# Kernel tuning notes

Hardware: AMD Instinct MI355X
Metric: run time of the kernel (lower is better)

Reference implementation:

```python
import jax, jax.numpy as jnp
import numpy as np

B, T, D = 64, 512, 256
K = 8192  # num_embeddings


def setup_inputs() -> dict:
    key = jax.random.key(0)
    k1, k2 = jax.random.split(key)
    inputs = jax.random.normal(k1, (B, T, D), dtype=jnp.float32)
    # nn.Embedding weight init: uniform(-1/K, 1/K)
    emb_weight = jax.random.uniform(k2, (K, D), dtype=jnp.float32, minval=-1.0 / K, maxval=1.0 / K)
    return {"inputs": inputs, "emb_weight": emb_weight}


def reference(inputs, emb_weight):
    d = emb_weight.shape[1]
    flat = inputs.reshape(-1, d)  # [N, D]
    # squared L2 distances to all codes: [N, K]
    distances = (
        jnp.sum(flat * flat, axis=1, keepdims=True)
        + jnp.sum(emb_weight * emb_weight, axis=1)
        - 2.0 * jnp.matmul(flat, emb_weight.T)
    )
    encoding_indices = jnp.argmin(distances, axis=1)  # [N]
    # one-hot @ codebook == direct gather of nearest code
    quantized = emb_weight[encoding_indices].reshape(inputs.shape)
    e_latent_loss = jnp.mean((jax.lax.stop_gradient(quantized) - inputs) ** 2)
    q_latent_loss = jnp.mean((quantized - jax.lax.stop_gradient(inputs)) ** 2)
    loss = q_latent_loss + e_latent_loss
    # straight-through estimator
    quantized_st = inputs + jax.lax.stop_gradient(quantized - inputs)
    return quantized_st, loss, encoding_indices.reshape(inputs.shape[0], -1)
```

## Files before the change

kernel.cpp:

```cpp
#include <hip/hip_runtime.h>

#define N_ROWS 32768
#define DIM 256
#define N_CODES 8192
#define OUT_Q 8388608
#define OUT_LOSS 8388608
#define OUT_IDX 8388609
#define FLAG_GAP 7e-5f
#define CAND_CAP 262144

#define WS_AROW 0
#define WS_IDX  131072
#define WS_LIST 262144
#define WS_CNT  393216
#define WS_CCNT 393232
#define WS_S1   393472
#define WS_KEYS 524544
#define WS_PART 524544
#define WS_EIMG 1048576

typedef __attribute__((ext_vector_type(8))) short short8x;
typedef __attribute__((ext_vector_type(4))) float f32x4;
typedef unsigned long long u64;
#define AS1 __attribute__((address_space(1)))
#define AS3 __attribute__((address_space(3)))

__device__ __forceinline__ u64 umin64(u64 a, u64 b) { return a < b ? a : b; }
__device__ __forceinline__ u64 umax64(u64 a, u64 b) { return a > b ? a : b; }
__device__ __forceinline__ unsigned fkey(float f) {
    unsigned b = __float_as_uint(f);
    return b ^ (unsigned)(((int)b >> 31) | 0x80000000);
}
__device__ __forceinline__ float fkeyinv(unsigned u) {
    unsigned b = (u >> 31) ? (u ^ 0x80000000u) : ~u;
    return __uint_as_float(b);
}
__device__ __forceinline__ unsigned short bf16rne(float f) {
    unsigned u = __float_as_uint(f);
    return (unsigned short)((u + 0x7fff + ((u >> 16) & 1)) >> 16);
}
__device__ __forceinline__ void gload16(const void* g, void* l) {
    __builtin_amdgcn_global_load_lds((const AS1 unsigned int*)g, (AS3 unsigned int*)l, 16, 0, 0);
}

__global__ void vq_prepE(const float* __restrict__ E, char* __restrict__ Eimg) {
    int t = blockIdx.x * 256 + threadIdx.x;
    int cb = t >> 10;
    int u = t & 1023;
    int w = u >> 7, v = u & 127;
    int sub = v >> 5, c = (v >> 4) & 1, l15 = v & 15;
    int tile = cb >> 3, S = cb & 7;
    const float* src = E + (size_t)(tile * 256 + w * 32 + c * 16 + l15) * DIM + S * 32 + sub * 8;
    unsigned short h[8], l[8];
#pragma unroll
    for (int j = 0; j < 8; ++j) {
        float vv = src[j];
        h[j] = bf16rne(vv);
        float hf = __uint_as_float((unsigned)h[j] << 16);
        l[j] = bf16rne(vv - hf);
    }
    short8x H, L;
#pragma unroll
    for (int j = 0; j < 8; ++j) { H[j] = (short)h[j]; L[j] = (short)l[j]; }
    char* dst = Eimg + (size_t)cb * 32768 + w * 4096 + sub * 512 + c * 256 + l15 * 16;
    *(short8x*)dst = H;
    *(short8x*)(dst + 2048) = L;
}

__global__ void vq_rowA(const float* __restrict__ X, float* __restrict__ Arow) {
    int row = blockIdx.x * 4 + (threadIdx.x >> 6);
    int lane = threadIdx.x & 63;
    const float4 v = *((const float4*)(X + (size_t)row * DIM + lane * 4));
    double s = (double)v.x * v.x + (double)v.y * v.y + (double)v.z * v.z + (double)v.w * v.w;
#pragma unroll
    for (int m = 1; m < 64; m <<= 1) s += __shfl_xor(s, m, 64);
    if (lane == 0) Arow[row] = (float)s;
}

template <int MODE>
__global__ __launch_bounds__(512, 1) void vq_scan(
    const float* __restrict__ X, const char* __restrict__ Eimg,
    const float* __restrict__ Arow, int* __restrict__ ws_idx,
    int* __restrict__ flaglist, int* __restrict__ flagcnt,
    u64* __restrict__ keybuf, float* __restrict__ s1buf,
    unsigned* __restrict__ cand, int* __restrict__ candcnt) {
    __shared__ alignas(16) unsigned short Xs[32768];
    __shared__ alignas(16) unsigned short Eb[32768];
    __shared__ int rows_s[64];

    const int tid = threadIdx.x;
    const int lane = tid & 63, wv = tid >> 6;
    const int l15 = lane & 15, sub = lane >> 4;

    const int cnt = (MODE == 1) ? *flagcnt : 0;
    const int ntasks = (MODE == 1) ? ((cnt + 63) >> 6) * 8 : 0;

    char* const ebase = (char*)Eb + wv * 4096;
    const char* const eimgw = Eimg + wv * 4096;

    float r1v[4][4], r2v[4][4];
    int c1v[4][4];
    if constexpr (MODE == 0) {
#pragma unroll
        for (int f = 0; f < 4; ++f)
#pragma unroll
            for (int g = 0; g < 4; ++g) { r1v[f][g] = 3.4e38f; r2v[f][g] = 3.4e38f; c1v[f][g] = 0; }
    }

    int task = blockIdx.x;
    while (true) {
        int t0, t1, r0;
        if constexpr (MODE == 1) {
            if (task >= ntasks) break;
            int grp = task >> 3;
            int rng = task & 7;
            t0 = rng * 4; t1 = t0 + 4;
            r0 = 0;
            __syncthreads();
            if (tid < 64) {
                int s = grp * 64 + tid;
                rows_s[tid] = flaglist[s < cnt ? s : cnt - 1];
            }
            __syncthreads();
        } else {
            t0 = 0; t1 = 32;
            r0 = blockIdx.x * 64;
        }
        const int cend = t1 * 8;

        {
            const int ci = t0 * 8;
            const char* src = eimgw + (size_t)ci * 32768 + lane * 16;
            char* dst = ebase + (ci & 1) * 32768;
#pragma unroll
            for (int i = 0; i < 4; ++i) gload16(src + i * 1024, dst + i * 1024);
        }
#pragma unroll
        for (int i = 0; i < 4; ++i) {
            int ci = tid + i * 512;
            int q = ci >> 6, r = ci & 63;
            int grow = (MODE == 1) ? rows_s[r] : r0 + r;
            const float* src = X + (size_t)grow * DIM + q * 8;
            unsigned short h[8], l[8];
#pragma unroll
            for (int j = 0; j < 8; ++j) {
                float v = src[j];
                h[j] = bf16rne(v);
                float hf = __uint_as_float((unsigned)h[j] << 16);
                l[j] = bf16rne(v - hf);
            }
            short8x H, L;
#pragma unroll
            for (int j = 0; j < 8; ++j) { H[j] = (short)h[j]; L[j] = (short)l[j]; }
            *(short8x*)((char*)Xs + q * 1024 + r * 16) = H;
            *(short8x*)((char*)Xs + 32768 + q * 1024 + r * 16) = L;
        }

        float A_r[4][4], s1v[4][4];
        int rid[4][4];
#pragma unroll
        for (int f = 0; f < 4; ++f)
#pragma unroll
            for (int g = 0; g < 4; ++g) {
                int rr = (MODE == 1) ? rows_s[f * 16 + sub * 4 + g] : r0 + f * 16 + sub * 4 + g;
                A_r[f][g] = Arow[rr];
                if constexpr (MODE == 1) { s1v[f][g] = s1buf[rr]; rid[f][g] = rr; }
            }

        __syncthreads();

        for (int t = t0; t < t1; ++t) {
            f32x4 acc[4][2];
#pragma unroll
            for (int f = 0; f < 4; ++f)
#pragma unroll
                for (int c = 0; c < 2; ++c) acc[f][c] = (f32x4){0.f, 0.f, 0.f, 0.f};

#pragma unroll
            for (int S = 0; S < 8; ++S) {
                const int ci = t * 8 + S;
                if (ci + 1 < cend) {
                    const char* src = eimgw + (size_t)(ci + 1) * 32768 + lane * 16;
                    char* dst = ebase + ((ci + 1) & 1) * 32768;
#pragma unroll
                    for (int i = 0; i < 4; ++i) gload16(src + i * 1024, dst + i * 1024);
                    __builtin_amdgcn_sched_barrier(0);
                    asm volatile("s_waitcnt vmcnt(4)" ::: "memory");
                } else {
                    asm volatile("s_waitcnt vmcnt(0)" ::: "memory");
                }
                __builtin_amdgcn_sched_barrier(0);

                const char* xb = (const char*)Xs;
                const char* eb = ebase + (ci & 1) * 32768;
                short8x ah[4], al[4], ehh[2], ell[2];
#pragma unroll
                for (int f = 0; f < 4; ++f) {
                    int off = (S * 4 + sub) * 1024 + f * 256 + l15 * 16;
                    ah[f] = *(const short8x*)(xb + off);
                    al[f] = *(const short8x*)(xb + 32768 + off);
                }
#pragma unroll
                for (int c = 0; c < 2; ++c) {
                    int off = sub * 512 + c * 256 + l15 * 16;
                    ehh[c] = *(const short8x*)(eb + off);
                    ell[c] = *(const short8x*)(eb + 2048 + off);
                }
#pragma unroll
                for (int f = 0; f < 4; ++f)
#pragma unroll
                    for (int c = 0; c < 2; ++c) {
                        f32x4 a = acc[f][c];
                        a = __builtin_amdgcn_mfma_f32_16x16x32_bf16(al[f], ehh[c], a, 0, 0, 0);
                        a = __builtin_amdgcn_mfma_f32_16x16x32_bf16(ah[f], ell[c], a, 0, 0, 0);
                        a = __builtin_amdgcn_mfma_f32_16x16x32_bf16(ah[f], ehh[c], a, 0, 0, 0);
                        acc[f][c] = a;
                    }
            }

            const int cbase = t * 256 + wv * 32 + l15;
            if constexpr (MODE == 0) {
#pragma unroll
                for (int f = 0; f < 4; ++f)
#pragma unroll
                    for (int g = 0; g < 4; ++g) {
                        float v0 = fmaf(-2.0f, acc[f][0][g], A_r[f][g]);
                        float v1 = fmaf(-2.0f, acc[f][1][g], A_r[f][g]);
                        float tt1 = fminf(v0, v1), tt2 = fmaxf(v0, v1);
                        int tc1 = (v1 < v0) ? cbase + 16 : cbase;
                        bool upd = (tt1 < r1v[f][g]);
                        r2v[f][g] = upd ? fminf(r1v[f][g], tt2) : fminf(r2v[f][g], tt1);
                        c1v[f][g] = upd ? tc1 : c1v[f][g];
                        r1v[f][g] = upd ? tt1 : r1v[f][g];
                    }
            } else {
#pragma unroll
                for (int f = 0; f < 4; ++f)
#pragma unroll
                    for (int g = 0; g < 4; ++g) {
                        float thr = s1v[f][g] + FLAG_GAP;
#pragma unroll
                        for (int c = 0; c < 2; ++c) {
                            float v = fmaf(-2.0f, acc[f][c][g], A_r[f][g]);
                            if (v <= thr) {
                                int slot = atomicAdd(candcnt, 1);
                                if (slot < CAND_CAP)
                                    cand[slot] = ((unsigned)rid[f][g] << 13) |
                                                 (unsigned)(cbase + c * 16);
                            }
                        }
                    }
            }
        }

        if constexpr (MODE == 0) break;
        else task += gridDim.x;
    }

    if constexpr (MODE == 0) {
        __syncthreads();
        u64* red = (u64*)Xs;
#pragma unroll
        for (int f = 0; f < 4; ++f)
#pragma unroll
            for (int g = 0; g < 4; ++g) {
                u64 k1 = ((u64)fkey(r1v[f][g]) << 32) | (unsigned)c1v[f][g];
                u64 k2 = ((u64)fkey(r2v[f][g]) << 32);
#pragma unroll
                for (int m = 1; m < 16; m <<= 1) {
                    u64 o1 = __shfl_xor(k1, m, 64);
                    u64 o2 = __shfl_xor(k2, m, 64);
                    u64 mx = umax64(k1, o1);
                    k1 = umin64(k1, o1);
                    k2 = umin64(umin64(k2, o2), mx);
                }
                if (l15 == 0) {
                    int row64 = f * 16 + sub * 4 + g;
                    red[(wv * 64 + row64) * 2 + 0] = k1;
                    red[(wv * 64 + row64) * 2 + 1] = k2;
                }
            }
        __syncthreads();
        if (tid < 64) {
            u64 K1 = red[tid * 2 + 0], K2 = red[tid * 2 + 1];
#pragma unroll
            for (int w = 1; w < 8; ++w) {
                u64 o1 = red[(w * 64 + tid) * 2 + 0], o2 = red[(w * 64 + tid) * 2 + 1];
                u64 mx = umax64(K1, o1);
                K1 = umin64(K1, o1);
                K2 = umin64(umin64(K2, o2), mx);
            }
            int r = blockIdx.x * 64 + tid;
            ws_idx[r] = (int)(unsigned)(K1 & 0xffffffffull);
            float s1 = fkeyinv((unsigned)(K1 >> 32));
            float s2 = fkeyinv((unsigned)(K2 >> 32));
            s1buf[r] = s1;
            if (s2 - s1 < FLAG_GAP) {
                keybuf[r] = ~0ull;
                int slot = atomicAdd(flagcnt, 1);
                flaglist[slot] = r;
            }
        }
    }
}

__global__ void vq_refine_cand(const float* __restrict__ X, const float* __restrict__ E,
                               const float* __restrict__ Arow, u64* __restrict__ keybuf,
                               const unsigned* __restrict__ cand,
                               const int* __restrict__ candcnt) {
    int cnt2 = *candcnt;
    cnt2 = cnt2 < CAND_CAP ? cnt2 : CAND_CAP;
    const int gw = (blockIdx.x * 256 + threadIdx.x) >> 6;
    const int nw = gridDim.x * 4;
    const int lane = threadIdx.x & 63;
    for (int i = gw; i < cnt2; i += nw) {
        unsigned p = cand[i];
        int row = (int)(p >> 13), code = (int)(p & 8191);
        float4 xv = *(const float4*)(X + (size_t)row * DIM + lane * 4);
        float4 ev = *(const float4*)(E + (size_t)code * DIM + lane * 4);
        double s = (double)xv.x * ev.x + (double)xv.y * ev.y +
                   (double)xv.z * ev.z + (double)xv.w * ev.w;
#pragma unroll
        for (int m = 1; m < 64; m <<= 1) s += __shfl_xor(s, m, 64);
        if (lane == 0) {
            float m32 = (float)s;
            float scr = fmaf(-2.0f, m32, Arow[row]);
            u64 key = ((u64)fkey(scr) << 32) | (unsigned)code;
            atomicMin(keybuf + row, key);
        }
    }
}

__global__ void vq_apply(const u64* __restrict__ keybuf, const int* __restrict__ flaglist,
                         const int* __restrict__ flagcnt, int* __restrict__ ws_idx) {
    int s = blockIdx.x * 256 + threadIdx.x;
    if (s < *flagcnt) {
        int r = flaglist[s];
        u64 k = keybuf[r];
        if (k != ~0ull) ws_idx[r] = (int)(unsigned)(k & 0xffffffffull);
    }
}

__global__ void vq_out(const float* __restrict__ X, const float* __restrict__ E,
                       const int* __restrict__ ws_idx, float* __restrict__ out,
                       float* __restrict__ partials) {
    const int r = (blockIdx.x * 256 + threadIdx.x) >> 6;
    const int lane = threadIdx.x & 63;
    int idx = ws_idx[r];
    idx = idx < 0 ? 0 : (idx > N_CODES - 1 ? N_CODES - 1 : idx);
    float4 e = *((const float4*)(E + (size_t)idx * DIM + lane * 4));
    float4 x = *((const float4*)(X + (size_t)r * DIM + lane * 4));
    float dx = e.x - x.x, dy = e.y - x.y, dz = e.z - x.z, dw = e.w - x.w;
    float4 o;
    o.x = x.x + dx; o.y = x.y + dy; o.z = x.z + dz; o.w = x.w + dw;
    *((float4*)(out + (size_t)r * DIM + lane * 4)) = o;
    float s = dx * dx + dy * dy + dz * dz + dw * dw;
#pragma unroll
    for (int m = 1; m < 64; m <<= 1) s += __shfl_xor(s, m, 64);
    if (lane == 0) {
        partials[r] = s;
        out[OUT_IDX + r] = (float)idx;
    }
}

__global__ void vq_loss(const float* __restrict__ partials, float* __restrict__ out) {
    __shared__ double sred[4];
    double s = 0.0;
    for (int i = threadIdx.x; i < N_ROWS; i += 256) s += (double)partials[i];
#pragma unroll
    for (int m = 1; m < 64; m <<= 1) s += __shfl_xor(s, m, 64);
    if ((threadIdx.x & 63) == 0) sred[threadIdx.x >> 6] = s;
    __syncthreads();
    if (threadIdx.x == 0) {
        double t = sred[0] + sred[1] + sred[2] + sred[3];
        out[OUT_LOSS] = (float)(2.0 * t / (double)OUT_Q);
    }
}

extern "C" void kernel_launch(void* const* d_in, const int* in_sizes, int n_in,
                              void* d_out, int out_size, void* d_ws, size_t ws_size,
                              hipStream_t stream) {
    const float* X = (const float*)d_in[0];
    const float* E = (const float*)d_in[1];
    float* out = (float*)d_out;
    char* ws = (char*)d_ws;

    float* Arow = (float*)(ws + WS_AROW);
    int* idx = (int*)(ws + WS_IDX);
    int* list = (int*)(ws + WS_LIST);
    int* cnt = (int*)(ws + WS_CNT);
    int* ccnt = (int*)(ws + WS_CCNT);
    float* s1buf = (float*)(ws + WS_S1);
    u64* keys = (u64*)(ws + WS_KEYS);
    float* part = (float*)(ws + WS_PART);
    char* eimg = (ws_size >= (size_t)(WS_EIMG + 8 * 1024 * 1024)) ? (ws + WS_EIMG) : (char*)d_out;
    unsigned* cand = (unsigned*)((char*)d_out + (16 << 20));

    hipMemsetAsync(ws + WS_CNT, 0, 32, stream);
    vq_prepE<<<1024, 256, 0, stream>>>(E, eimg);
    vq_rowA<<<N_ROWS / 4, 256, 0, stream>>>(X, Arow);
    vq_scan<0><<<N_ROWS / 64, 512, 0, stream>>>(X, eimg, Arow, idx, list, cnt, keys, s1buf,
                                                cand, ccnt);
    vq_scan<1><<<512, 512, 0, stream>>>(X, eimg, Arow, idx, list, cnt, keys, s1buf, cand, ccnt);
    vq_refine_cand<<<1024, 256, 0, stream>>>(X, E, Arow, keys, cand, ccnt);
    vq_apply<<<128, 256, 0, stream>>>(keys, list, cnt, idx);
    vq_out<<<N_ROWS / 4, 256, 0, stream>>>(X, E, idx, out, part);
    vq_loss<<<1, 256, 0, stream>>>(part, out);
}
```

Before: 542.8 us.

## Load codebook fragments directly into registers instead of staging through LDS

The codebook image is re-laid out so each lane's MFMA B-operand fragment is contiguous. Each wave then reads its fragments from global memory straight into registers, with a one-step register prefetch in place of global_load_lds double buffering. This removes the 64KB LDS buffer, the LDS reads and the explicit vmcnt waits. In exchange, global load latency is hidden only by the compiler's scheduling of one chunk ahead, and register pressure goes up.

```diff
diff --git a/kernel.cpp b/kernel.cpp
--- a/kernel.cpp
+++ b/kernel.cpp
@@ -22,8 +22,6 @@
 typedef __attribute__((ext_vector_type(8))) short short8x;
 typedef __attribute__((ext_vector_type(4))) float f32x4;
 typedef unsigned long long u64;
-#define AS1 __attribute__((address_space(1)))
-#define AS3 __attribute__((address_space(3)))
 
 __device__ __forceinline__ u64 umin64(u64 a, u64 b) { return a < b ? a : b; }
 __device__ __forceinline__ u64 umax64(u64 a, u64 b) { return a > b ? a : b; }
@@ -39,18 +37,18 @@
     unsigned u = __float_as_uint(f);
     return (unsigned short)((u + 0x7fff + ((u >> 16) & 1)) >> 16);
 }
-__device__ __forceinline__ void gload16(const void* g, void* l) {
-    __builtin_amdgcn_global_load_lds((const AS1 unsigned int*)g, (AS3 unsigned int*)l, 16, 0, 0);
-}
 
 __global__ void vq_prepE(const float* __restrict__ E, char* __restrict__ Eimg) {
     int t = blockIdx.x * 256 + threadIdx.x;
-    int cb = t >> 10;
+    int ci = t >> 10;
     int u = t & 1023;
-    int w = u >> 7, v = u & 127;
-    int sub = v >> 5, c = (v >> 4) & 1, l15 = v & 15;
-    int tile = cb >> 3, S = cb & 7;
-    const float* src = E + (size_t)(tile * 256 + w * 32 + c * 16 + l15) * DIM + S * 32 + sub * 8;
+    int wv = u >> 7;
+    int v = u & 127;
+    int c = v >> 6, lane = v & 63;
+    int tile = ci >> 3, S = ci & 7;
+    int code = tile * 256 + wv * 32 + c * 16 + (lane & 15);
+    int k0 = S * 32 + (lane >> 4) * 8;
+    const float* src = E + (size_t)code * DIM + k0;
     unsigned short h[8], l[8];
 #pragma unroll
     for (int j = 0; j < 8; ++j) {
@@ -62,7 +60,7 @@
     short8x H, L;
 #pragma unroll
     for (int j = 0; j < 8; ++j) { H[j] = (short)h[j]; L[j] = (short)l[j]; }
-    char* dst = Eimg + (size_t)cb * 32768 + w * 4096 + sub * 512 + c * 256 + l15 * 16;
+    char* dst = Eimg + (size_t)ci * 32768 + wv * 4096 + c * 1024 + lane * 16;
     *(short8x*)dst = H;
     *(short8x*)(dst + 2048) = L;
 }
@@ -85,7 +83,6 @@
     u64* __restrict__ keybuf, float* __restrict__ s1buf,
     unsigned* __restrict__ cand, int* __restrict__ candcnt) {
     __shared__ alignas(16) unsigned short Xs[32768];
-    __shared__ alignas(16) unsigned short Eb[32768];
     __shared__ int rows_s[64];
 
     const int tid = threadIdx.x;
@@ -95,8 +92,7 @@
     const int cnt = (MODE == 1) ? *flagcnt : 0;
     const int ntasks = (MODE == 1) ? ((cnt + 63) >> 6) * 8 : 0;
 
-    char* const ebase = (char*)Eb + wv * 4096;
-    const char* const eimgw = Eimg + wv * 4096;
+    const char* const eimgw = Eimg + wv * 4096 + lane * 16;
 
     float r1v[4][4], r2v[4][4];
     int c1v[4][4];
@@ -128,12 +124,13 @@
         }
         const int cend = t1 * 8;
 
+        short8x pnh0, pnh1, pnl0, pnl1;
         {
-            const int ci = t0 * 8;
-            const char* src = eimgw + (size_t)ci * 32768 + lane * 16;
-            char* dst = ebase + (ci & 1) * 32768;
-#pragma unroll
-            for (int i = 0; i < 4; ++i) gload16(src + i * 1024, dst + i * 1024);
+            const char* p = eimgw + (size_t)(t0 * 8) * 32768;
+            pnh0 = *(const short8x*)p;
+            pnh1 = *(const short8x*)(p + 1024);
+            pnl0 = *(const short8x*)(p + 2048);
+            pnl1 = *(const short8x*)(p + 3072);
         }
 #pragma unroll
         for (int i = 0; i < 4; ++i) {
@@ -179,21 +176,17 @@
 #pragma unroll
             for (int S = 0; S < 8; ++S) {
                 const int ci = t * 8 + S;
+                short8x eh0 = pnh0, eh1 = pnh1, el0 = pnl0, el1 = pnl1;
                 if (ci + 1 < cend) {
-                    const char* src = eimgw + (size_t)(ci + 1) * 32768 + lane * 16;
-                    char* dst = ebase + ((ci + 1) & 1) * 32768;
-#pragma unroll
-                    for (int i = 0; i < 4; ++i) gload16(src + i * 1024, dst + i * 1024);
-                    __builtin_amdgcn_sched_barrier(0);
-                    asm volatile("s_waitcnt vmcnt(4)" ::: "memory");
-                } else {
-                    asm volatile("s_waitcnt vmcnt(0)" ::: "memory");
-                }
-                __builtin_amdgcn_sched_barrier(0);
+                    const char* p = eimgw + (size_t)(ci + 1) * 32768;
+                    pnh0 = *(const short8x*)p;
+                    pnh1 = *(const short8x*)(p + 1024);
+                    pnl0 = *(const short8x*)(p + 2048);
+                    pnl1 = *(const short8x*)(p + 3072);
+                }
 
                 const char* xb = (const char*)Xs;
-                const char* eb = ebase + (ci & 1) * 32768;
-                short8x ah[4], al[4], ehh[2], ell[2];
+                short8x ah[4], al[4];
 #pragma unroll
                 for (int f = 0; f < 4; ++f) {
                     int off = (S * 4 + sub) * 1024 + f * 256 + l15 * 16;
@@ -201,21 +194,18 @@
                     al[f] = *(const short8x*)(xb + 32768 + off);
                 }
 #pragma unroll
-                for (int c = 0; c < 2; ++c) {
-                    int off = sub * 512 + c * 256 + l15 * 16;
-                    ehh[c] = *(const short8x*)(eb + off);
-                    ell[c] = *(const short8x*)(eb + 2048 + off);
-                }
-#pragma unroll
-                for (int f = 0; f < 4; ++f)
-#pragma unroll
-                    for (int c = 0; c < 2; ++c) {
-                        f32x4 a = acc[f][c];
-                        a = __builtin_amdgcn_mfma_f32_16x16x32_bf16(al[f], ehh[c], a, 0, 0, 0);
-                        a = __builtin_amdgcn_mfma_f32_16x16x32_bf16(ah[f], ell[c], a, 0, 0, 0);
-                        a = __builtin_amdgcn_mfma_f32_16x16x32_bf16(ah[f], ehh[c], a, 0, 0, 0);
-                        acc[f][c] = a;
-                    }
+                for (int f = 0; f < 4; ++f) {
+                    f32x4 a0 = acc[f][0];
+                    a0 = __builtin_amdgcn_mfma_f32_16x16x32_bf16(al[f], eh0, a0, 0, 0, 0);
+                    a0 = __builtin_amdgcn_mfma_f32_16x16x32_bf16(ah[f], el0, a0, 0, 0, 0);
+                    a0 = __builtin_amdgcn_mfma_f32_16x16x32_bf16(ah[f], eh0, a0, 0, 0, 0);
+                    acc[f][0] = a0;
+                    f32x4 a1 = acc[f][1];
+                    a1 = __builtin_amdgcn_mfma_f32_16x16x32_bf16(al[f], eh1, a1, 0, 0, 0);
+                    a1 = __builtin_amdgcn_mfma_f32_16x16x32_bf16(ah[f], el1, a1, 0, 0, 0);
+                    a1 = __builtin_amdgcn_mfma_f32_16x16x32_bf16(ah[f], eh1, a1, 0, 0, 0);
+                    acc[f][1] = a1;
+                }
             }
 
             const int cbase = t * 256 + wv * 32 + l15;
```

Result: slower. 1.195 ms (+120.1%).

## Track top-3 in scan to shrink the rescan list for ambiguous rows

Applied to the files above, without the earlier changes.

The first scan now keeps the best three distances per row, together with the indices of the best two. For rows with a small top-2 gap it pushes both candidates straight into the refine list. Only rows whose third-best is also within a gap threshold go to the second (full-codebook) rescan, which should cut the number of rows rescanned. The rescan task split is also refined from 8 to 16 code ranges per row group. The cost is more registers and compare logic in the hot scan loop, and a heuristic gap threshold that could miss a true nearest code.

```diff
diff --git a/kernel.cpp b/kernel.cpp
--- a/kernel.cpp
+++ b/kernel.cpp
@@ -7,13 +7,13 @@
 #define OUT_LOSS 8388608
 #define OUT_IDX 8388609
 #define FLAG_GAP 7e-5f
+#define GAP3 1e-4f
 #define CAND_CAP 262144
 
 #define WS_AROW 0
 #define WS_IDX  131072
 #define WS_LIST 262144
 #define WS_CNT  393216
-#define WS_CCNT 393232
 #define WS_S1   393472
 #define WS_KEYS 524544
 #define WS_PART 524544
@@ -26,7 +26,6 @@
 #define AS3 __attribute__((address_space(3)))
 
 __device__ __forceinline__ u64 umin64(u64 a, u64 b) { return a < b ? a : b; }
-__device__ __forceinline__ u64 umax64(u64 a, u64 b) { return a > b ? a : b; }
 __device__ __forceinline__ unsigned fkey(float f) {
     unsigned b = __float_as_uint(f);
     return b ^ (unsigned)(((int)b >> 31) | 0x80000000);
@@ -41,6 +40,15 @@
 }
 __device__ __forceinline__ void gload16(const void* g, void* l) {
     __builtin_amdgcn_global_load_lds((const AS1 unsigned int*)g, (AS3 unsigned int*)l, 16, 0, 0);
+}
+__device__ __forceinline__ void triple_merge(u64& k1, u64& k2, u64& k3, u64 o1, u64 o2, u64 o3) {
+    bool c = o1 < k1;
+    u64 A1 = c ? o1 : k1, A2 = c ? o2 : k2, A3 = c ? o3 : k3;
+    u64 B1 = c ? k1 : o1, B2 = c ? k2 : o2;
+    bool d = B1 < A2;
+    k1 = A1;
+    k2 = d ? B1 : A2;
+    k3 = d ? umin64(A2, B2) : umin64(A3, B1);
 }
 
 __global__ void vq_prepE(const float* __restrict__ E, char* __restrict__ Eimg) {
@@ -83,7 +91,8 @@
     const float* __restrict__ Arow, int* __restrict__ ws_idx,
     int* __restrict__ flaglist, int* __restrict__ flagcnt,
     u64* __restrict__ keybuf, float* __restrict__ s1buf,
-    unsigned* __restrict__ cand, int* __restrict__ candcnt) {
+    unsigned* __restrict__ cand, int* __restrict__ candcnt,
+    int* __restrict__ list2, int* __restrict__ cnt2) {
     __shared__ alignas(16) unsigned short Xs[32768];
     __shared__ alignas(16) unsigned short Eb[32768];
     __shared__ int rows_s[64];
@@ -93,18 +102,21 @@
     const int l15 = lane & 15, sub = lane >> 4;
 
     const int cnt = (MODE == 1) ? *flagcnt : 0;
-    const int ntasks = (MODE == 1) ? ((cnt + 63) >> 6) * 8 : 0;
+    const int ntasks = (MODE == 1) ? ((cnt + 63) >> 6) * 16 : 0;
 
     char* const ebase = (char*)Eb + wv * 4096;
     const char* const eimgw = Eimg + wv * 4096;
 
-    float r1v[4][4], r2v[4][4];
-    int c1v[4][4];
+    float r1v[4][4], r2v[4][4], r3v[4][4];
+    int c1v[4][4], c2v[4][4];
     if constexpr (MODE == 0) {
 #pragma unroll
         for (int f = 0; f < 4; ++f)
 #pragma unroll
-            for (int g = 0; g < 4; ++g) { r1v[f][g] = 3.4e38f; r2v[f][g] = 3.4e38f; c1v[f][g] = 0; }
+            for (int g = 0; g < 4; ++g) {
+                r1v[f][g] = 3.4e38f; r2v[f][g] = 3.4e38f; r3v[f][g] = 3.4e38f;
+                c1v[f][g] = 0; c2v[f][g] = 0;
+            }
     }
 
     int task = blockIdx.x;
@@ -112,9 +124,9 @@
         int t0, t1, r0;
         if constexpr (MODE == 1) {
             if (task >= ntasks) break;
-            int grp = task >> 3;
-            int rng = task & 7;
-            t0 = rng * 4; t1 = t0 + 4;
+            int grp = task >> 4;
+            int rng = task & 15;
+            t0 = rng * 2; t1 = t0 + 2;
             r0 = 0;
             __syncthreads();
             if (tid < 64) {
@@ -226,12 +238,23 @@
                     for (int g = 0; g < 4; ++g) {
                         float v0 = fmaf(-2.0f, acc[f][0][g], A_r[f][g]);
                         float v1 = fmaf(-2.0f, acc[f][1][g], A_r[f][g]);
-                        float tt1 = fminf(v0, v1), tt2 = fmaxf(v0, v1);
-                        int tc1 = (v1 < v0) ? cbase + 16 : cbase;
-                        bool upd = (tt1 < r1v[f][g]);
-                        r2v[f][g] = upd ? fminf(r1v[f][g], tt2) : fminf(r2v[f][g], tt1);
-                        c1v[f][g] = upd ? tc1 : c1v[f][g];
-                        r1v[f][g] = upd ? tt1 : r1v[f][g];
+                        bool sw = v1 < v0;
+                        float lo = sw ? v1 : v0, hi = sw ? v0 : v1;
+                        int ilo = sw ? cbase + 16 : cbase;
+                        int ihi = sw ? cbase : cbase + 16;
+                        bool cond = lo < r1v[f][g];
+                        float A2 = cond ? hi : r2v[f][g];
+                        float A3 = cond ? 3.4e38f : r3v[f][g];
+                        float B1 = cond ? r1v[f][g] : lo;
+                        float B2 = cond ? r2v[f][g] : hi;
+                        int iA2 = cond ? ihi : c2v[f][g];
+                        int iB1 = cond ? c1v[f][g] : ilo;
+                        r1v[f][g] = cond ? lo : r1v[f][g];
+                        c1v[f][g] = cond ? ilo : c1v[f][g];
+                        bool d = B1 < A2;
+                        r2v[f][g] = d ? B1 : A2;
+                        c2v[f][g] = d ? iB1 : iA2;
+                        r3v[f][g] = d ? fminf(A2, B2) : fminf(A3, B1);
                     }
             } else {
 #pragma unroll
@@ -265,40 +288,47 @@
 #pragma unroll
             for (int g = 0; g < 4; ++g) {
                 u64 k1 = ((u64)fkey(r1v[f][g]) << 32) | (unsigned)c1v[f][g];
-                u64 k2 = ((u64)fkey(r2v[f][g]) << 32);
+                u64 k2 = ((u64)fkey(r2v[f][g]) << 32) | (unsigned)c2v[f][g];
+                u64 k3 = ((u64)fkey(r3v[f][g]) << 32) | 0x1fffu;
 #pragma unroll
                 for (int m = 1; m < 16; m <<= 1) {
                     u64 o1 = __shfl_xor(k1, m, 64);
                     u64 o2 = __shfl_xor(k2, m, 64);
-                    u64 mx = umax64(k1, o1);
-                    k1 = umin64(k1, o1);
-                    k2 = umin64(umin64(k2, o2), mx);
+                    u64 o3 = __shfl_xor(k3, m, 64);
+                    triple_merge(k1, k2, k3, o1, o2, o3);
                 }
                 if (l15 == 0) {
                     int row64 = f * 16 + sub * 4 + g;
-                    red[(wv * 64 + row64) * 2 + 0] = k1;
-                    red[(wv * 64 + row64) * 2 + 1] = k2;
+                    red[(wv * 64 + row64) * 3 + 0] = k1;
+                    red[(wv * 64 + row64) * 3 + 1] = k2;
+                    red[(wv * 64 + row64) * 3 + 2] = k3;
                 }
             }
         __syncthreads();
         if (tid < 64) {
-            u64 K1 = red[tid * 2 + 0], K2 = red[tid * 2 + 1];
+            u64 K1 = red[tid * 3 + 0], K2 = red[tid * 3 + 1], K3 = red[tid * 3 + 2];
 #pragma unroll
             for (int w = 1; w < 8; ++w) {
-                u64 o1 = red[(w * 64 + tid) * 2 + 0], o2 = red[(w * 64 + tid) * 2 + 1];
-                u64 mx = umax64(K1, o1);
-                K1 = umin64(K1, o1);
-                K2 = umin64(umin64(K2, o2), mx);
+                triple_merge(K1, K2, K3,
+                             red[(w * 64 + tid) * 3 + 0],
+                             red[(w * 64 + tid) * 3 + 1],
+                             red[(w * 64 + tid) * 3 + 2]);
             }
             int r = blockIdx.x * 64 + tid;
             ws_idx[r] = (int)(unsigned)(K1 & 0xffffffffull);
             float s1 = fkeyinv((unsigned)(K1 >> 32));
             float s2 = fkeyinv((unsigned)(K2 >> 32));
+            float s3 = fkeyinv((unsigned)(K3 >> 32));
             s1buf[r] = s1;
             if (s2 - s1 < FLAG_GAP) {
                 keybuf[r] = ~0ull;
-                int slot = atomicAdd(flagcnt, 1);
-                flaglist[slot] = r;
+                flaglist[atomicAdd(flagcnt, 1)] = r;
+                int cs = atomicAdd(candcnt, 2);
+                if (cs + 1 < CAND_CAP) {
+                    cand[cs]     = ((unsigned)r << 13) | (unsigned)(K1 & 8191ull);
+                    cand[cs + 1] = ((unsigned)r << 13) | (unsigned)(K2 & 8191ull);
+                }
+                if (s3 - s1 <= GAP3) list2[atomicAdd(cnt2, 1)] = r;
             }
         }
     }
@@ -389,19 +419,22 @@
     int* idx = (int*)(ws + WS_IDX);
     int* list = (int*)(ws + WS_LIST);
     int* cnt = (int*)(ws + WS_CNT);
-    int* ccnt = (int*)(ws + WS_CCNT);
+    int* cnt2 = (int*)(ws + WS_CNT + 8);
+    int* ccnt = (int*)(ws + WS_CNT + 16);
     float* s1buf = (float*)(ws + WS_S1);
     u64* keys = (u64*)(ws + WS_KEYS);
     float* part = (float*)(ws + WS_PART);
     char* eimg = (ws_size >= (size_t)(WS_EIMG + 8 * 1024 * 1024)) ? (ws + WS_EIMG) : (char*)d_out;
     unsigned* cand = (unsigned*)((char*)d_out + (16 << 20));
+    int* list2 = (int*)((char*)d_out + (17 << 20));
 
     hipMemsetAsync(ws + WS_CNT, 0, 32, stream);
     vq_prepE<<<1024, 256, 0, stream>>>(E, eimg);
     vq_rowA<<<N_ROWS / 4, 256, 0, stream>>>(X, Arow);
     vq_scan<0><<<N_ROWS / 64, 512, 0, stream>>>(X, eimg, Arow, idx, list, cnt, keys, s1buf,
-                                                cand, ccnt);
-    vq_scan<1><<<512, 512, 0, stream>>>(X, eimg, Arow, idx, list, cnt, keys, s1buf, cand, ccnt);
+                                                cand, ccnt, list2, cnt2);
+    vq_scan<1><<<512, 512, 0, stream>>>(X, eimg, Arow, idx, list2, cnt2, keys, s1buf,
+                                        cand, ccnt, list2, cnt2);
     vq_refine_cand<<<1024, 256, 0, stream>>>(X, E, Arow, keys, cand, ccnt);
     vq_apply<<<128, 256, 0, stream>>>(keys, list, cnt, idx);
     vq_out<<<N_ROWS / 4, 256, 0, stream>>>(X, E, idx, out, part);
```

Result: faster. 500.0 us (-7.9%).
